# Performance work log

Measured on AMD Instinct MI355X. Metric: run time of the kernel, lower is better.

The kernel has to match this reference:

```python
import jax, jax.numpy as jnp
import numpy as np

D = 256          # feature_dim
H = 4            # num_heads (hard-coded in AdaAttentionalPropagation)
HD = D // H      # per-head dim = 64
L = 6            # number of layers
B, N, M = 2, 2048, 2048
NAMES = ("self", "cross", "self", "cross", "self", "cross")
POOLS = (1, 1, 2, 2, 2, 2)
EPS = 1e-5


def conv1x1(W, b, x):
    # Conv1d kernel_size=1 == pointwise linear over channels: x [B, Cin, N] -> [B, Cout, N]
    return jnp.einsum('oi,bin->bon', W, x) + b[None, :, None]


def inst_norm(x):
    # InstanceNorm1d(affine=False): normalize over spatial dim per (batch, channel)
    mu = jnp.mean(x, axis=-1, keepdims=True)
    var = jnp.var(x, axis=-1, keepdims=True)
    return (x - mu) * jax.lax.rsqrt(var + EPS)


def attn_prop(params, x, source, mask):
    # One AdaAttentionalPropagation layer. x [B,D,Nq], source [B,D,Nk], mask [B,Nq,Nk]
    Wq, bq, Wk, bk, Wv, bv, Wm, bm, W1, b1, W2, b2 = params
    b = x.shape[0]
    q = conv1x1(Wq, bq, x).reshape(b, HD, H, -1)       # [B, hd, H, Nq]
    k = conv1x1(Wk, bk, source).reshape(b, HD, H, -1)  # [B, hd, H, Nk]
    v = conv1x1(Wv, bv, source).reshape(b, HD, H, -1)
    scores = jnp.einsum('bdhn,bdhm->bhnm', q, k) / np.sqrt(HD).astype(np.float32)
    scores = scores * mask[:, None]                     # multiplicative pruned mask
    prob = jax.nn.softmax(scores, axis=-1)              # [B, H, Nq, Nk]
    att = jnp.einsum('bhnm,bdhm->bdhn', prob, v).reshape(b, D, -1)
    message = conv1x1(Wm, bm, att)                      # merge
    y = jnp.concatenate([x, message], axis=1)           # [B, 2D, Nq]
    h = jax.nn.relu(inst_norm(conv1x1(W1, b1, y)))      # MLP_IN hidden
    delta = conv1x1(W2, b2, h)                          # [B, D, Nq]
    return delta, jnp.mean(prob, axis=1)                # prob averaged over heads


def prune(conn, prob, pool, k_cur):
    # update_connections_by_pooling_size: keep top (k_cur // pool) entries per row
    if prob is None or pool == 1:
        return conn, k_cur
    k_new = k_cur // pool
    vals, idxs = jax.lax.top_k(prob, k_new)             # over last axis
    b, n, _ = conn.shape
    new = jnp.zeros_like(conn).at[
        jnp.arange(b)[:, None, None], jnp.arange(n)[None, :, None], idxs
    ].set(jnp.where(vals > 0, 1.0, 0.0).astype(conn.dtype))
    return jax.lax.stop_gradient(new), k_new


def setup_inputs() -> dict:
    key = jax.random.key(0)
    ks = jax.random.split(key, 16)
    s1 = 1.0 / np.sqrt(D)
    s2 = 1.0 / np.sqrt(2 * D)
    return {
        "desc0": jax.random.normal(ks[0], (B, D, N), dtype=jnp.float32),
        "desc1": jax.random.normal(ks[1], (B, D, M), dtype=jnp.float32),
        "Wq": jax.random.normal(ks[2], (L, D, D), dtype=jnp.float32) * s1,
        "bq": jax.random.normal(ks[3], (L, D), dtype=jnp.float32) * 0.01,
        "Wk": jax.random.normal(ks[4], (L, D, D), dtype=jnp.float32) * s1,
        "bk": jax.random.normal(ks[5], (L, D), dtype=jnp.float32) * 0.01,
        "Wv": jax.random.normal(ks[6], (L, D, D), dtype=jnp.float32) * s1,
        "bv": jax.random.normal(ks[7], (L, D), dtype=jnp.float32) * 0.01,
        "Wm": jax.random.normal(ks[8], (L, D, D), dtype=jnp.float32) * s1,
        "bm": jax.random.normal(ks[9], (L, D), dtype=jnp.float32) * 0.01,
        "W1": jax.random.normal(ks[10], (L, 2 * D, 2 * D), dtype=jnp.float32) * s2,
        "b1": jax.random.normal(ks[11], (L, 2 * D), dtype=jnp.float32) * 0.01,
        "W2": jax.random.normal(ks[12], (L, D, 2 * D), dtype=jnp.float32) * s2,
        "b2": jnp.zeros((L, D), dtype=jnp.float32),  # nn.init.constant_(mlp[-1].bias, 0)
    }


def reference(desc0, desc1, Wq, bq, Wk, bk, Wv, bv, Wm, bm, W1, b1, W2, b2):
    b = desc0.shape[0]
    n, m = desc0.shape[2], desc1.shape[2]
    masks = {
        '00': jnp.ones((b, n, n), jnp.float32), '01': jnp.ones((b, n, m), jnp.float32),
        '11': jnp.ones((b, m, m), jnp.float32), '10': jnp.ones((b, m, n), jnp.float32),
    }
    probs = {'00': None, '01': None, '11': None, '10': None}
    kcnt = {'00': n, '01': m, '11': m, '10': n}
    for i in range(L):
        params = (Wq[i], bq[i], Wk[i], bk[i], Wv[i], bv[i],
                  Wm[i], bm[i], W1[i], b1[i], W2[i], b2[i])
        pool = POOLS[i]
        if NAMES[i] == 'cross':
            masks['01'], kcnt['01'] = prune(masks['01'], probs['01'], pool, kcnt['01'])
            delta0, probs['01'] = attn_prop(params, desc0, desc1, masks['01'])
            masks['10'], kcnt['10'] = prune(masks['10'], probs['10'], pool, kcnt['10'])
            delta1, probs['10'] = attn_prop(params, desc1, desc0, masks['10'])
        else:
            masks['00'], kcnt['00'] = prune(masks['00'], probs['00'], pool, kcnt['00'])
            delta0, probs['00'] = attn_prop(params, desc0, desc0, masks['00'])
            masks['11'], kcnt['11'] = prune(masks['11'], probs['11'], pool, kcnt['11'])
            delta1, probs['11'] = attn_prop(params, desc1, desc1, masks['11'])
        desc0 = desc0 + delta0
        desc1 = desc1 + delta1
    return jnp.stack([desc0, desc1])  # [2, B, D, N]
```

## Files before the change

kernel.cpp:

```cpp
#include <hip/hip_runtime.h>
#include <hip/hip_bf16.h>
#include <stdint.h>

#define NPTS 2048
#define MB_ROW 256L
#define MB_B   ((long)NPTS * MB_ROW)
#define MB_T   (2 * MB_B)

typedef __attribute__((ext_vector_type(8))) short bf16x8;
typedef __attribute__((ext_vector_type(4))) float f32x4;
#define MFMA16 __builtin_amdgcn_mfma_f32_16x16x32_bf16

__device__ inline unsigned short f2b(float f) {
  union { float f; unsigned int u; } x; x.f = f;
  unsigned int u = x.u;
  return (unsigned short)((u + 0x7FFFu + ((u >> 16) & 1u)) >> 16);
}
__device__ inline float bfu(unsigned int us) {
  union { unsigned int u; float f; } x; x.u = (us & 0xFFFFu) << 16;
  return x.f;
}
__device__ inline void sp3(float x, unsigned short& h, unsigned short& m, unsigned short& l) {
  h = f2b(x);
  float r1 = x - bfu(h);
  m = f2b(r1);
  l = f2b(r1 - bfu(m));
}
__device__ inline void gld16(const unsigned short* g, unsigned short* l) {
  __builtin_amdgcn_global_load_lds(
      (const __attribute__((address_space(1))) void*)g,
      (__attribute__((address_space(3))) void*)l, 16, 0, 0);
}

#define E_P3  0
#define E_V3  1
#define E_S3  2
#define E_Y3  3
#define E_H   4
#define E_RES 5

template <int EPI>
__global__ __launch_bounds__(256) void t3_k(
    const unsigned short* __restrict__ A, long aps,
    const unsigned short* __restrict__ B, long bps,
    const unsigned short* __restrict__ B2, long b2ps,
    const float* __restrict__ bias,
    void* __restrict__ out,
    const unsigned char* __restrict__ masks,
    int K, int lda, int ldb, int ksplit, long sps,
    int zbase, int xorv, int selfl, int yoff) {
  const int t = threadIdx.x;
  const int z = blockIdx.z;
  const int zg = zbase + z;
  long aoff = 0, boff = 0, b2off = 0;
  if constexpr (EPI == E_P3 || EPI == E_V3) {
    boff = (long)z * 524288;
  } else if constexpr (EPI == E_S3) {
    const int sb = zg >> 2, h = zg & 3;
    aoff = (long)zg * 131072;
    boff = (long)((sb ^ xorv) * 4 + h) * 131072;
  } else if constexpr (EPI == E_Y3) {
    boff = (long)zg * 524288;
  } else if constexpr (EPI == E_H) {
    boff = (long)zg * 524288;
    b2off = (long)z * 524288;
  } else {
    boff = (long)z * 1048576;
  }
  const int n0 = blockIdx.x * 64;
  const int m0 = ((EPI == E_S3) ? yoff : 0) + blockIdx.y * 64;

  __shared__ __align__(16) unsigned short As[3][64 * 64];
  __shared__ __align__(16) unsigned short Bs[3][64 * 64];
  __shared__ unsigned int Ms[128];
  if constexpr (EPI == E_S3) {
    if (t < 128) {
      const int sb = zg >> 2;
      const int type = selfl ? (sb >> 1) : 2 + (sb >> 1);
      const unsigned int* mw =
          (const unsigned int*)(masks + (long)type * MB_T + (long)(sb & 1) * MB_B);
      Ms[t] = mw[(long)(m0 + (t >> 1)) * 64 + (n0 >> 5) + (t & 1)];
    }
  }

  const int w = t >> 6;
  const int L = t & 63;
  const int wm = (w & 1) * 32, wn = (w >> 1) * 32;
  const int lr = t & 15, lk = (t >> 4) & 3;
  const int swr = (lr & 7) << 3;
  const int grow = (L >> 3);
  const int gj = L & 7;

  f32x4 acc[2][2];
#pragma unroll
  for (int i = 0; i < 2; ++i)
#pragma unroll
    for (int j = 0; j < 2; ++j) acc[i][j] = (f32x4){0.f, 0.f, 0.f, 0.f};

  for (int k0 = 0; k0 < K; k0 += 64) {
    const unsigned short* Bsel;
    long bo, bp;
    int kb;
    if (k0 < ksplit) { Bsel = B; bo = boff; bp = bps; kb = k0; }
    else             { Bsel = B2; bo = b2off; bp = b2ps; kb = k0 - ksplit; }
    if (k0) __syncthreads();
#pragma unroll
    for (int pl = 0; pl < 3; ++pl) {
      const unsigned short* Ap = A + (long)pl * aps + aoff;
      const unsigned short* Bp = Bsel + (long)pl * bp + bo;
#pragma unroll
      for (int c = 0; c < 2; ++c) {
        const int rbase = w * 16 + c * 8;
        const int row = rbase + grow;
        const int colA = (gj ^ (row & 7)) << 3;
        gld16(&Ap[(long)(m0 + row) * lda + k0 + colA], &As[pl][rbase * 64]);
        gld16(&Bp[(long)(n0 + row) * ldb + kb + colA], &Bs[pl][rbase * 64]);
      }
    }
    __syncthreads();
#pragma unroll
    for (int kk = 0; kk < 2; ++kk) {
      bf16x8 af[3][2], bf[3][2];
#pragma unroll
      for (int pl = 0; pl < 3; ++pl)
#pragma unroll
        for (int mi = 0; mi < 2; ++mi) {
          af[pl][mi] = *(const bf16x8*)&As[pl][(wm + mi * 16 + lr) * 64 + ((kk * 32 + lk * 8) ^ swr)];
          bf[pl][mi] = *(const bf16x8*)&Bs[pl][(wn + mi * 16 + lr) * 64 + ((kk * 32 + lk * 8) ^ swr)];
        }
#pragma unroll
      for (int mi = 0; mi < 2; ++mi)
#pragma unroll
        for (int ni = 0; ni < 2; ++ni) {
          f32x4 c = acc[mi][ni];
          c = MFMA16(af[2][mi], bf[0][ni], c, 0, 0, 0);
          c = MFMA16(af[0][mi], bf[2][ni], c, 0, 0, 0);
          c = MFMA16(af[1][mi], bf[1][ni], c, 0, 0, 0);
          c = MFMA16(af[1][mi], bf[0][ni], c, 0, 0, 0);
          c = MFMA16(af[0][mi], bf[1][ni], c, 0, 0, 0);
          c = MFMA16(af[0][mi], bf[0][ni], c, 0, 0, 0);
          acc[mi][ni] = c;
        }
    }
  }

  if constexpr (EPI == E_S3) {
    __syncthreads();
    float* ST = (float*)&As[0][0];
#pragma unroll
    for (int mi = 0; mi < 2; ++mi)
#pragma unroll
      for (int ni = 0; ni < 2; ++ni)
#pragma unroll
        for (int r = 0; r < 4; ++r)
          ST[(wm + mi * 16 + lk * 4 + r) * 68 + wn + ni * 16 + lr] = acc[mi][ni][r];
    __syncthreads();
    float* o = (float*)out;
#pragma unroll
    for (int it = 0; it < 4; ++it) {
      const int row = (t >> 4) + it * 16;
      const int col = (t & 15) * 4;
      float4 vv = *(const float4*)&ST[row * 68 + col];
      const unsigned int mw = Ms[row * 2 + (col >> 5)];
      vv.x = ((mw >> ((col + 0) & 31)) & 1u) ? vv.x * 0.125f : 0.f;
      vv.y = ((mw >> ((col + 1) & 31)) & 1u) ? vv.y * 0.125f : 0.f;
      vv.z = ((mw >> ((col + 2) & 31)) & 1u) ? vv.z * 0.125f : 0.f;
      vv.w = ((mw >> ((col + 3) & 31)) & 1u) ? vv.w * 0.125f : 0.f;
      const int rloc = blockIdx.y * 64 + row;
      *(float4*)&o[(long)z * sps + (long)rloc * 2048 + n0 + col] = vv;
    }
    return;
  }

#pragma unroll
  for (int mi = 0; mi < 2; ++mi) {
#pragma unroll
    for (int ni = 0; ni < 2; ++ni) {
      f32x4 a = acc[mi][ni];
      const int cM = m0 + wm + mi * 16 + lk * 4;
      const int pN = n0 + wn + ni * 16 + lr;
      if constexpr (EPI == E_P3) {
        float4 bv4 = *(const float4*)&bias[cM];
        float bb[4] = {bv4.x, bv4.y, bv4.z, bv4.w};
        unsigned short* o = (unsigned short*)out;
        const long b0 = (long)z * 524288 + (long)pN * 64 + (cM >> 2);
#pragma unroll
        for (int r = 0; r < 4; ++r) {
          unsigned short h_, m_, l_;
          sp3(a[r] + bb[r], h_, m_, l_);
          const long ad = b0 + (long)r * 131072;
          o[ad] = h_; o[ad + 2097152] = m_; o[ad + 4194304] = l_;
        }
      } else if constexpr (EPI == E_V3) {
        float4 bv4 = *(const float4*)&bias[cM];
        float bb[4] = {bv4.x, bv4.y, bv4.z, bv4.w};
        unsigned short* o = (unsigned short*)out;
        const long b0 = (long)z * 524288 + (long)(cM >> 2) * 2048 + pN;
#pragma unroll
        for (int r = 0; r < 4; ++r) {
          unsigned short h_, m_, l_;
          sp3(a[r] + bb[r], h_, m_, l_);
          const long ad = b0 + (long)r * 131072;
          o[ad] = h_; o[ad + 2097152] = m_; o[ad + 4194304] = l_;
        }
      } else if constexpr (EPI == E_Y3) {
        float4 bv4 = *(const float4*)&bias[cM];
        float bb[4] = {bv4.x, bv4.y, bv4.z, bv4.w};
        unsigned short* o = (unsigned short*)out;
        ushort4 h4, m4, l4;
        unsigned short* hp = (unsigned short*)&h4;
        unsigned short* mp = (unsigned short*)&m4;
        unsigned short* lp = (unsigned short*)&l4;
#pragma unroll
        for (int r = 0; r < 4; ++r) sp3(a[r] + bb[r], hp[r], mp[r], lp[r]);
        const long b0 = (long)z * 524288 + (long)pN * 256 + cM;
        *(ushort4*)&o[b0] = h4;
        *(ushort4*)&o[b0 + sps] = m4;
        *(ushort4*)&o[b0 + 2 * sps] = l4;
      } else if constexpr (EPI == E_H) {
        *(f32x4*)&((float*)out)[(long)z * 1048576 + (long)pN * 512 + cM] = a;
      } else {
        float4 bv4 = *(const float4*)&bias[cM];
        float* p = &((float*)out)[(long)zg * 524288 + (long)pN * 256 + cM];
        float4 old = *(const float4*)p;
        float4 nw;
        nw.x = old.x + a[0] + bv4.x; nw.y = old.y + a[1] + bv4.y;
        nw.z = old.z + a[2] + bv4.z; nw.w = old.w + a[3] + bv4.w;
        *(float4*)p = nw;
      }
    }
  }
}

__global__ __launch_bounds__(256) void pv3_k(
    const unsigned short* __restrict__ V3, const float* __restrict__ S, long sps,
    const float2* __restrict__ stats, int CH,
    float* __restrict__ part, int zbase, int xorv) {
  const int t = threadIdx.x;
  const int h = blockIdx.z;
  const int kseg = blockIdx.y;
  const int n0 = blockIdx.x * 64;
  const int sb = zbase >> 2;
  const unsigned short* Vb = V3 + (long)((sb ^ xorv) * 4 + h) * 131072;
  const float* Sp = S + (long)h * sps;
  const float2* sth = stats + (long)h * CH;

  __shared__ __align__(16) unsigned short Bs[3][64 * 64];

  const int w = t >> 6;
  const int wm = (w & 1) * 32, wn = (w >> 1) * 32;
  const int lr = t & 15, lk = (t >> 4) & 3;
  const int srow = t >> 3, scol = (t & 7) * 8;
  const int sws = scol ^ ((srow & 7) << 3);
  const int swr = (lr & 7) << 3;

  f32x4 acc[2][2];
#pragma unroll
  for (int i = 0; i < 2; ++i)
#pragma unroll
    for (int j = 0; j < 2; ++j) acc[i][j] = (f32x4){0.f, 0.f, 0.f, 0.f};

  const int kbeg = kseg * 256;
  const float2 st0 = sth[n0 + srow];
  const float2 st1 = sth[n0 + 32 + srow];
  const float* srcA = &Sp[(long)(n0 + srow) * 2048 + kbeg + scol];
  const float* srcB = &Sp[(long)(n0 + 32 + srow) * 2048 + kbeg + scol];

  float4 c0a = *(const float4*)srcA;
  float4 c0b = *(const float4*)(srcA + 4);
  float4 c1a = *(const float4*)srcB;
  float4 c1b = *(const float4*)(srcB + 4);

#pragma unroll
  for (int ki = 0; ki < 4; ++ki) {
    const int k0 = kbeg + ki * 64;
    float4 n0a, n0b, n1a, n1b;
    if (ki < 3) {
      const int off = (ki + 1) * 64;
      n0a = *(const float4*)(srcA + off);
      n0b = *(const float4*)(srcA + off + 4);
      n1a = *(const float4*)(srcB + off);
      n1b = *(const float4*)(srcB + off + 4);
    }
    if (ki) __syncthreads();
    {
      float xs[8] = {c0a.x, c0a.y, c0a.z, c0a.w, c0b.x, c0b.y, c0b.z, c0b.w};
      ushort4 hq[2], mq[2], lq[2];
      unsigned short* hp = (unsigned short*)hq;
      unsigned short* mp = (unsigned short*)mq;
      unsigned short* lp = (unsigned short*)lq;
#pragma unroll
      for (int j = 0; j < 8; ++j) {
        float p = __expf(xs[j] - st0.x) * st0.y;
        sp3(p, hp[j], mp[j], lp[j]);
      }
      *(ushort4*)&Bs[0][srow * 64 + sws] = hq[0];
      *(ushort4*)&Bs[0][srow * 64 + sws + 4] = hq[1];
      *(ushort4*)&Bs[1][srow * 64 + sws] = mq[0];
      *(ushort4*)&Bs[1][srow * 64 + sws + 4] = mq[1];
      *(ushort4*)&Bs[2][srow * 64 + sws] = lq[0];
      *(ushort4*)&Bs[2][srow * 64 + sws + 4] = lq[1];
    }
    {
      float xs[8] = {c1a.x, c1a.y, c1a.z, c1a.w, c1b.x, c1b.y, c1b.z, c1b.w};
      ushort4 hq[2], mq[2], lq[2];
      unsigned short* hp = (unsigned short*)hq;
      unsigned short* mp = (unsigned short*)mq;
      unsigned short* lp = (unsigned short*)lq;
#pragma unroll
      for (int j = 0; j < 8; ++j) {
        float p = __expf(xs[j] - st1.x) * st1.y;
        sp3(p, hp[j], mp[j], lp[j]);
      }
      const int rr = 32 + srow;
      *(ushort4*)&Bs[0][rr * 64 + sws] = hq[0];
      *(ushort4*)&Bs[0][rr * 64 + sws + 4] = hq[1];
      *(ushort4*)&Bs[1][rr * 64 + sws] = mq[0];
      *(ushort4*)&Bs[1][rr * 64 + sws + 4] = mq[1];
      *(ushort4*)&Bs[2][rr * 64 + sws] = lq[0];
      *(ushort4*)&Bs[2][rr * 64 + sws + 4] = lq[1];
    }
    __syncthreads();
#pragma unroll
    for (int kk = 0; kk < 2; ++kk) {
      bf16x8 af[3][2], bf[3][2];
#pragma unroll
      for (int pl = 0; pl < 3; ++pl) {
#pragma unroll
        for (int mi = 0; mi < 2; ++mi) {
          af[pl][mi] = *(const bf16x8*)&Vb[(long)pl * 2097152 +
                                           (long)(wm + mi * 16 + lr) * 2048 + k0 + kk * 32 + lk * 8];
          bf[pl][mi] = *(const bf16x8*)&Bs[pl][(wn + mi * 16 + lr) * 64 + ((kk * 32 + lk * 8) ^ swr)];
        }
      }
#pragma unroll
      for (int mi = 0; mi < 2; ++mi)
#pragma unroll
        for (int ni = 0; ni < 2; ++ni) {
          f32x4 c = acc[mi][ni];
          c = MFMA16(af[2][mi], bf[0][ni], c, 0, 0, 0);
          c = MFMA16(af[0][mi], bf[2][ni], c, 0, 0, 0);
          c = MFMA16(af[1][mi], bf[1][ni], c, 0, 0, 0);
          c = MFMA16(af[1][mi], bf[0][ni], c, 0, 0, 0);
          c = MFMA16(af[0][mi], bf[1][ni], c, 0, 0, 0);
          c = MFMA16(af[0][mi], bf[0][ni], c, 0, 0, 0);
          acc[mi][ni] = c;
        }
    }
    if (ki < 3) { c0a = n0a; c0b = n0b; c1a = n1a; c1b = n1b; }
  }

  float* pp = part + (((long)kseg * 4 + h) * CH) * 64;
#pragma unroll
  for (int mi = 0; mi < 2; ++mi) {
#pragma unroll
    for (int ni = 0; ni < 2; ++ni) {
      const int cM = wm + mi * 16 + lk * 4;
      const int pN = n0 + wn + ni * 16 + lr;
      *(f32x4*)&pp[(long)pN * 64 + cM] = acc[mi][ni];
    }
  }
}

__global__ __launch_bounds__(256) void comb_k(const float* __restrict__ part,
                                              unsigned short* __restrict__ att3,
                                              int CH, int sb, int cb) {
  const int q = threadIdx.x & 63;
  const int g = threadIdx.x >> 6;
  const int nl = blockIdx.x * 4 + g;
  float s[4] = {0.f, 0.f, 0.f, 0.f};
#pragma unroll
  for (int ks = 0; ks < 8; ++ks)
#pragma unroll
    for (int h = 0; h < 4; ++h)
      s[h] += part[(((long)ks * 4 + h) * CH + nl) * 64 + q];
  ushort4 h4, m4, l4;
  unsigned short* hp = (unsigned short*)&h4;
  unsigned short* mp = (unsigned short*)&m4;
  unsigned short* lp = (unsigned short*)&l4;
#pragma unroll
  for (int h = 0; h < 4; ++h) sp3(s[h], hp[h], mp[h], lp[h]);
  const long base = (long)sb * 524288 + (long)(cb + nl) * 256 + 4 * q;
  *(ushort4*)&att3[base] = h4;
  *(ushort4*)&att3[base + 2097152] = m4;
  *(ushort4*)&att3[base + 4194304] = l4;
}

template <int PRUNE>
__global__ __launch_bounds__(256) void softmax_prune_k(
    const float* __restrict__ S, float2* __restrict__ stats,
    unsigned char* __restrict__ masks,
    int knew, int sbG, int cb, int selfl, long sps, int CH) {
  const int lane = threadIdx.x & 63;
  const int wv = threadIdx.x >> 6;
  const int nl = blockIdx.x * 4 + wv;

  __shared__ float meanL[PRUNE ? 4 * 32 * 64 : 1];
  __shared__ int hist[PRUNE ? 4 * 256 : 4];
  float* myMean = PRUNE ? &meanL[(wv * 32) * 64 + lane] : nullptr;

  if constexpr (PRUNE) {
#pragma unroll
    for (int j = 0; j < 32; ++j) myMean[j * 64] = 0.f;
  }

  float mx4[4], ri4[4];
#pragma unroll
  for (int hh = 0; hh < 4; ++hh) {
    const float* row = S + (long)hh * sps + (long)nl * 2048 + lane * 32;
    float xs[32];
#pragma unroll
    for (int e = 0; e < 8; ++e) {
      float4 u = *(const float4*)(row + e * 4);
      xs[e * 4 + 0] = u.x; xs[e * 4 + 1] = u.y;
      xs[e * 4 + 2] = u.z; xs[e * 4 + 3] = u.w;
    }
    float m = xs[0];
#pragma unroll
    for (int j = 1; j < 32; ++j) m = fmaxf(m, xs[j]);
    for (int o = 32; o; o >>= 1) m = fmaxf(m, __shfl_xor(m, o));
    float s = 0.f;
#pragma unroll
    for (int j = 0; j < 32; ++j) { xs[j] = __expf(xs[j] - m); s += xs[j]; }
    for (int o = 32; o; o >>= 1) s += __shfl_xor(s, o);
    const float ri = 1.0f / s;
    mx4[hh] = m; ri4[hh] = ri;
    if constexpr (PRUNE) {
#pragma unroll
      for (int j = 0; j < 32; ++j)
        myMean[j * 64] += 0.25f * (xs[j] * ri);
    }
  }
  if (lane == 0) {
#pragma unroll
    for (int hh = 0; hh < 4; ++hh)
      stats[(long)hh * CH + nl] = make_float2(mx4[hh], ri4[hh]);
  }

  if constexpr (PRUNE) {
    unsigned int key[32];
#pragma unroll
    for (int j = 0; j < 32; ++j) key[j] = __float_as_uint(myMean[j * 64]);

    int* hw = &hist[wv * 256];
    unsigned int pref = 0;
    int kneed = knew;
    for (int pass = 0; pass < 4; ++pass) {
      const int shift = 24 - pass * 8;
      const unsigned int hm = (pass == 0) ? 0u : (0xFFFFFFFFu << (shift + 8));
#pragma unroll
      for (int b = 0; b < 4; ++b) hw[b * 64 + lane] = 0;
      __syncthreads();
#pragma unroll
      for (int j = 0; j < 32; ++j)
        if ((key[j] & hm) == pref) atomicAdd(&hw[(key[j] >> shift) & 255], 1);
      __syncthreads();
      int own[4];
      int tot = 0;
#pragma unroll
      for (int e = 0; e < 4; ++e) { own[e] = hw[lane * 4 + e]; tot += own[e]; }
      int suf = tot;
      for (int o = 1; o < 64; o <<= 1) {
        int tmp = __shfl_down(suf, o);
        if (lane + o < 64) suf += tmp;
      }
      int run = suf - tot;
      int pack = 0;
#pragma unroll
      for (int e = 3; e >= 0; --e) {
        const int Sb = run + own[e];
        if (Sb >= kneed && run < kneed) pack = ((lane * 4 + e) << 20) | (run + 1);
        run = Sb;
      }
      for (int o = 1; o < 64; o <<= 1) pack |= __shfl_xor(pack, o);
      const int bin = pack >> 20;
      const int above = (pack & 0xFFFFF) - 1;
      pref |= ((unsigned int)bin) << shift;
      kneed -= above;
    }
    const unsigned int T = pref;
    const int take = kneed;
    int cnt = 0;
#pragma unroll
    for (int j = 0; j < 32; ++j) cnt += (key[j] == T);
    int pc = cnt;
    for (int o = 1; o < 64; o <<= 1) {
      int tmp = __shfl_up(pc, o);
      if (lane >= o) pc += tmp;
    }
    int base = pc - cnt;
    uchar4 ob;
    unsigned char* obp = (unsigned char*)&ob;
#pragma unroll
    for (int byte = 0; byte < 4; ++byte) {
      unsigned int bb = 0;
#pragma unroll
      for (int e = 0; e < 8; ++e) {
        const int j = byte * 8 + e;
        int sel = 0;
        if (key[j] > T) sel = 1;
        else if (key[j] == T) { if (T > 0u && base < take) sel = 1; base++; }
        bb |= (unsigned int)sel << e;
      }
      obp[byte] = (unsigned char)bb;
    }
    const int type = selfl ? (sbG >> 1) : 2 + (sbG >> 1);
    unsigned char* mb = masks + (long)type * MB_T + (long)(sbG & 1) * MB_B;
    *(uchar4*)&mb[(long)(cb + nl) * MB_ROW + lane * 4] = ob;
  }
}

__global__ __launch_bounds__(256) void inormA_k(const float* __restrict__ H,
                                                float* __restrict__ partial) {
  const int seg = blockIdx.x, sbl = blockIdx.y;
  const float* hp = H + (long)sbl * 1048576;
  const int t = threadIdx.x;
  float s0 = 0.f, q0 = 0.f, s1 = 0.f, q1 = 0.f;
  const int r0 = seg * 64;
  for (int r = r0; r < r0 + 64; ++r) {
    float x0 = hp[(long)r * 512 + t];
    float x1 = hp[(long)r * 512 + t + 256];
    s0 += x0; q0 = fmaf(x0, x0, q0);
    s1 += x1; q1 = fmaf(x1, x1, q1);
  }
  float* pp = partial + ((long)sbl * 32 + seg) * 1024;
  pp[t] = s0; pp[t + 256] = s1;
  pp[512 + t] = q0; pp[512 + t + 256] = q1;
}

__global__ __launch_bounds__(256) void inormB_k(const float* __restrict__ partial,
                                                float* __restrict__ stats2) {
  const int sbl = blockIdx.x;
  const int t = threadIdx.x;
  const float* pp = partial + (long)sbl * 32768;
  float a0 = 0.f, b0 = 0.f, a1 = 0.f, b1 = 0.f;
  for (int seg = 0; seg < 32; ++seg) {
    const float* p = pp + seg * 1024;
    a0 += p[t]; a1 += p[t + 256];
    b0 += p[512 + t]; b1 += p[512 + t + 256];
  }
  float mu0 = a0 * (1.f / 2048.f);
  float mu1 = a1 * (1.f / 2048.f);
  float rs0 = rsqrtf(b0 * (1.f / 2048.f) - mu0 * mu0 + 1e-5f);
  float rs1 = rsqrtf(b1 * (1.f / 2048.f) - mu1 * mu1 + 1e-5f);
  float* st = stats2 + (long)sbl * 1024;
  st[t] = mu0; st[t + 256] = mu1;
  st[512 + t] = rs0; st[512 + t + 256] = rs1;
}

__global__ __launch_bounds__(256) void inormC_k(const float* __restrict__ H,
                                                const float* __restrict__ stats2,
                                                unsigned short* __restrict__ HB,
                                                long hps) {
  const int seg = blockIdx.x, sbl = blockIdx.y;
  const float* hp = H + (long)sbl * 1048576;
  unsigned short* hb = HB + (long)sbl * 1048576;
  const float* st = stats2 + (long)sbl * 1024;
  const int t = threadIdx.x;
  const float mu0 = st[t], mu1 = st[t + 256];
  const float rs0 = st[512 + t], rs1 = st[512 + t + 256];
  const int r0 = seg * 64;
  for (int r = r0; r < r0 + 64; ++r) {
    float x0 = hp[(long)r * 512 + t];
    float x1 = hp[(long)r * 512 + t + 256];
    float o0 = (x0 - mu0) * rs0; o0 = o0 > 0.f ? o0 : 0.f;
    float o1 = (x1 - mu1) * rs1; o1 = o1 > 0.f ? o1 : 0.f;
    unsigned short h_, m_, l_;
    sp3(o0, h_, m_, l_);
    const long ad0 = (long)r * 512 + t;
    hb[ad0] = h_; hb[ad0 + hps] = m_; hb[ad0 + 2 * hps] = l_;
    sp3(o1, h_, m_, l_);
    const long ad1 = ad0 + 256;
    hb[ad1] = h_; hb[ad1 + hps] = m_; hb[ad1 + 2 * hps] = l_;
  }
}

__global__ __launch_bounds__(256) void split6_k(
    const float* __restrict__ q, const float* __restrict__ k,
    const float* __restrict__ v, const float* __restrict__ m,
    const float* __restrict__ w1, const float* __restrict__ w2,
    unsigned short* __restrict__ dst) {
  long i = ((long)blockIdx.x * 256 + threadIdx.x) * 4;
  const float* src;
  long off, base, ps;
  if (i < 262144) {
    int sel = (int)(i >> 16);
    src = sel == 0 ? q : sel == 1 ? k : sel == 2 ? v : m;
    off = i & 65535; base = (long)sel * 196608; ps = 65536;
  } else if (i < 524288) {
    src = w1; off = i - 262144; base = 786432; ps = 262144;
  } else {
    src = w2; off = i - 524288; base = 1572864; ps = 131072;
  }
  float4 vv = *(const float4*)&src[off];
  float xs[4] = {vv.x, vv.y, vv.z, vv.w};
  ushort4 h4, m4, l4;
  unsigned short* hp = (unsigned short*)&h4;
  unsigned short* mp = (unsigned short*)&m4;
  unsigned short* lp = (unsigned short*)&l4;
#pragma unroll
  for (int j = 0; j < 4; ++j) sp3(xs[j], hp[j], mp[j], lp[j]);
  *(ushort4*)&dst[base + off] = h4;
  *(ushort4*)&dst[base + ps + off] = m4;
  *(ushort4*)&dst[base + 2 * ps + off] = l4;
}

__global__ __launch_bounds__(256) void split3_k(const float* __restrict__ src,
                                                unsigned short* __restrict__ dst,
                                                long plane, long n) {
  long i = ((long)blockIdx.x * 256 + threadIdx.x) * 4;
  if (i >= n) return;
  float4 v = *(const float4*)&src[i];
  float xs[4] = {v.x, v.y, v.z, v.w};
  ushort4 h4, m4, l4;
  unsigned short* hp = (unsigned short*)&h4;
  unsigned short* mp = (unsigned short*)&m4;
  unsigned short* lp = (unsigned short*)&l4;
#pragma unroll
  for (int j = 0; j < 4; ++j) sp3(xs[j], hp[j], mp[j], lp[j]);
  *(ushort4*)&dst[i] = h4;
  *(ushort4*)&dst[plane + i] = m4;
  *(ushort4*)&dst[2 * plane + i] = l4;
}

__global__ __launch_bounds__(256) void tin_k(const float* __restrict__ d0,
                                             const float* __restrict__ d1,
                                             float* __restrict__ descT) {
  __shared__ float tl[32][33];
  const int sb = blockIdx.z, s = sb >> 1, b = sb & 1;
  const float* src = (s ? d1 : d0) + (long)b * 524288;
  const int p0 = blockIdx.x * 32, c0 = blockIdx.y * 32;
  const int tx = threadIdx.x & 31, ty = threadIdx.x >> 5;
#pragma unroll
  for (int i = 0; i < 4; ++i)
    tl[ty + i * 8][tx] = src[(long)(c0 + ty + i * 8) * 2048 + p0 + tx];
  __syncthreads();
#pragma unroll
  for (int i = 0; i < 4; ++i)
    descT[(long)sb * 524288 + (long)(p0 + ty + i * 8) * 256 + c0 + tx] = tl[tx][ty + i * 8];
}

__global__ __launch_bounds__(256) void tout_k(const float* __restrict__ descT,
                                              float* __restrict__ out) {
  __shared__ float tl[32][33];
  const int sb = blockIdx.z;
  const int p0 = blockIdx.x * 32, c0 = blockIdx.y * 32;
  const int tx = threadIdx.x & 31, ty = threadIdx.x >> 5;
#pragma unroll
  for (int i = 0; i < 4; ++i)
    tl[ty + i * 8][tx] = descT[(long)sb * 524288 + (long)(p0 + ty + i * 8) * 256 + c0 + tx];
  __syncthreads();
#pragma unroll
  for (int i = 0; i < 4; ++i)
    out[(long)sb * 524288 + (long)(c0 + ty + i * 8) * 2048 + p0 + tx] = tl[tx][ty + i * 8];
}

extern "C" void kernel_launch(void* const* d_in, const int* in_sizes, int n_in,
                              void* d_out, int out_size, void* d_ws, size_t ws_size,
                              hipStream_t stream) {
  (void)in_sizes; (void)n_in; (void)out_size;
  const float* in_d0 = (const float*)d_in[0];
  const float* in_d1 = (const float*)d_in[1];
  const float* Wq = (const float*)d_in[2];
  const float* bq = (const float*)d_in[3];
  const float* Wk = (const float*)d_in[4];
  const float* bk = (const float*)d_in[5];
  const float* Wv = (const float*)d_in[6];
  const float* bv = (const float*)d_in[7];
  const float* Wm = (const float*)d_in[8];
  const float* bm = (const float*)d_in[9];
  const float* W1 = (const float*)d_in[10];
  const float* b1 = (const float*)d_in[11];
  const float* W2 = (const float*)d_in[12];
  const float* b2 = (const float*)d_in[13];
  (void)b1;

  const long region_b = (long)ws_size - 79429632;
  const int CH = (region_b >= 40992L * 2048) ? 2048
               : (region_b >= 40992L * 1024) ? 1024 : 512;
  const int nchunks = 2048 / CH;
  const long sps = (long)CH * 2048;
  const int mb = (region_b >= 4 * 13766656L) ? 4 : (region_b >= 2 * 13766656L) ? 2 : 1;

  uint8_t* w = (uint8_t*)d_ws;
  float* descT          = (float*)w;
  unsigned short* desc3 = (unsigned short*)(w + 8388608);
  unsigned short* Q3    = (unsigned short*)(w + 20971520);
  unsigned short* K3    = (unsigned short*)(w + 33554432);
  unsigned short* V3    = (unsigned short*)(w + 46137344);
  unsigned short* att3  = (unsigned short*)(w + 58720256);
  unsigned short* wbuf  = (unsigned short*)(w + 71303168);
  unsigned char* masks  = w + 75235328;
  uint8_t* region       = w + 79429632;
  float* S              = (float*)region;
  float* part           = (float*)(region + (long)CH * 32768);
  float2* stats         = (float2*)(region + (long)CH * 32768 + (long)CH * 8192);
  unsigned short* msg3  = (unsigned short*)region;
  float* hbuf           = (float*)(region + (long)mb * 3145728);
  unsigned short* hB3   = (unsigned short*)(region + (long)mb * 7340032);
  float* inpart         = (float*)(region + (long)mb * 13631488);
  float* instats        = (float*)(region + (long)mb * 13631488 + (long)mb * 131072);

  const unsigned short* wq3 = wbuf;
  const unsigned short* wk3 = wbuf + 196608;
  const unsigned short* wv3 = wbuf + 393216;
  const unsigned short* wm3 = wbuf + 589824;
  const unsigned short* w13 = wbuf + 786432;
  const unsigned short* w23 = wbuf + 1572864;

  tin_k<<<dim3(64, 8, 4), 256, 0, stream>>>(in_d0, in_d1, descT);
  hipMemsetAsync(masks, 0xFF, 4 * MB_T, stream);

  for (int l = 0; l < 6; ++l) {
    const int selfl = (l % 2 == 0);
    const int xorv = selfl ? 0 : 2;
    const int knew = (l < 2) ? 1024 : (l < 4) ? 512 : 0;

    split6_k<<<dim3(640), 256, 0, stream>>>(Wq + (long)l * 65536, Wk + (long)l * 65536,
                                            Wv + (long)l * 65536, Wm + (long)l * 65536,
                                            W1 + (long)l * 262144, W2 + (long)l * 131072,
                                            wbuf);
    split3_k<<<dim3(2048), 256, 0, stream>>>(descT, desc3, 2097152, 2097152);

    t3_k<E_P3><<<dim3(32, 4, 4), 256, 0, stream>>>(
        wq3, 65536, desc3, 2097152, nullptr, 0, bq + l * 256, Q3, nullptr,
        256, 256, 256, 1 << 30, 0, 0, 0, 0, 0);
    t3_k<E_P3><<<dim3(32, 4, 4), 256, 0, stream>>>(
        wk3, 65536, desc3, 2097152, nullptr, 0, bk + l * 256, K3, nullptr,
        256, 256, 256, 1 << 30, 0, 0, 0, 0, 0);
    t3_k<E_V3><<<dim3(32, 4, 4), 256, 0, stream>>>(
        wv3, 65536, desc3, 2097152, nullptr, 0, bv + l * 256, V3, nullptr,
        256, 256, 256, 1 << 30, 0, 0, 0, 0, 0);

    for (int sb = 0; sb < 4; ++sb) {
      for (int c = 0; c < nchunks; ++c) {
        const int cb = c * CH;
        t3_k<E_S3><<<dim3(32, CH / 64, 4), 256, 0, stream>>>(
            Q3, 2097152, K3, 2097152, nullptr, 0, nullptr, S, masks,
            64, 64, 64, 1 << 30, sps, sb * 4, xorv, selfl, cb);
        if (knew)
          softmax_prune_k<1><<<dim3(CH / 4), 256, 0, stream>>>(S, stats, masks, knew, sb, cb, selfl, sps, CH);
        else
          softmax_prune_k<0><<<dim3(CH / 4), 256, 0, stream>>>(S, stats, masks, knew, sb, cb, selfl, sps, CH);
        pv3_k<<<dim3(CH / 64, 8, 4), 256, 0, stream>>>(V3, S, sps, stats, CH, part, sb * 4, xorv);
        comb_k<<<dim3(CH / 4), 256, 0, stream>>>(part, att3, CH, sb, cb);
      }
    }

    for (int p = 0; p < 4; p += mb) {
      t3_k<E_Y3><<<dim3(32, 4, mb), 256, 0, stream>>>(
          wm3, 65536, att3, 2097152, nullptr, 0, bm + l * 256, msg3, nullptr,
          256, 256, 256, 1 << 30, (long)mb * 524288, p, 0, 0, 0);
      t3_k<E_H><<<dim3(32, 8, mb), 256, 0, stream>>>(
          w13, 262144, desc3, 2097152, msg3, (long)mb * 524288, nullptr, hbuf, nullptr,
          512, 512, 256, 256, 0, p, 0, 0, 0);
      inormA_k<<<dim3(32, mb), 256, 0, stream>>>(hbuf, inpart);
      inormB_k<<<dim3(mb), 256, 0, stream>>>(inpart, instats);
      inormC_k<<<dim3(32, mb), 256, 0, stream>>>(hbuf, instats, hB3, (long)mb * 1048576);
      t3_k<E_RES><<<dim3(32, 4, mb), 256, 0, stream>>>(
          w23, 131072, hB3, (long)mb * 1048576, nullptr, 0, b2 + l * 256, descT, nullptr,
          512, 512, 512, 1 << 30, 0, p, 0, 0, 0);
    }
  }

  tout_k<<<dim3(64, 8, 4), 256, 0, stream>>>(descT, (float*)d_out);
}
```

Before: 2.876 ms.

## Fuse per-tile softmax max/sum stats into score GEMM epilogue

The score GEMM epilogue now computes a per-row, per-64-column-tile max and exp-sum and writes them to a partial buffer that aliases the part scratch space. A small stat_k kernel merges these 32 partials into the row max and inverse sum. The separate softmax pass over S is removed for layers that do not prune, and the prune kernel reuses the precomputed stats. This saves a full read of S whenever no pruning happens, at the cost of extra shuffles and exp evaluations in the GEMM epilogue plus one added small launch.

```diff
diff --git a/kernel.cpp b/kernel.cpp
--- a/kernel.cpp
+++ b/kernel.cpp
@@ -156,6 +156,8 @@
           ST[(wm + mi * 16 + lk * 4 + r) * 68 + wn + ni * 16 + lr] = acc[mi][ni][r];
     __syncthreads();
     float* o = (float*)out;
+    float2* pst = (float2*)const_cast<float*>(bias);
+    const int CHrows = (int)(sps >> 11);
 #pragma unroll
     for (int it = 0; it < 4; ++it) {
       const int row = (t >> 4) + it * 16;
@@ -168,6 +170,15 @@
       vv.w = ((mw >> ((col + 3) & 31)) & 1u) ? vv.w * 0.125f : 0.f;
       const int rloc = blockIdx.y * 64 + row;
       *(float4*)&o[(long)z * sps + (long)rloc * 2048 + n0 + col] = vv;
+      float mx4 = fmaxf(fmaxf(vv.x, vv.y), fmaxf(vv.z, vv.w));
+#pragma unroll
+      for (int oo = 1; oo < 16; oo <<= 1) mx4 = fmaxf(mx4, __shfl_xor(mx4, oo));
+      float e4 = __expf(vv.x - mx4) + __expf(vv.y - mx4) +
+                 __expf(vv.z - mx4) + __expf(vv.w - mx4);
+#pragma unroll
+      for (int oo = 1; oo < 16; oo <<= 1) e4 += __shfl_xor(e4, oo);
+      if ((t & 15) == 0)
+        pst[((long)z * CHrows + rloc) * 32 + blockIdx.x] = make_float2(mx4, e4);
     }
     return;
   }
@@ -232,6 +243,19 @@
   }
 }
 
+__global__ __launch_bounds__(256) void stat_k(const float2* __restrict__ pst,
+                                              float2* __restrict__ stats) {
+  const int idx = blockIdx.x * 256 + threadIdx.x;
+  const float2* p = pst + (long)idx * 32;
+  float m = p[0].x;
+#pragma unroll
+  for (int i = 1; i < 32; ++i) m = fmaxf(m, p[i].x);
+  float s = 0.f;
+#pragma unroll
+  for (int i = 0; i < 32; ++i) s += p[i].y * __expf(p[i].x - m);
+  stats[idx] = make_float2(m, 1.0f / s);
+}
+
 __global__ __launch_bounds__(256) void pv3_k(
     const unsigned short* __restrict__ V3, const float* __restrict__ S, long sps,
     const float2* __restrict__ stats, int CH,
@@ -386,128 +410,104 @@
   *(ushort4*)&att3[base + 4194304] = l4;
 }
 
-template <int PRUNE>
-__global__ __launch_bounds__(256) void softmax_prune_k(
-    const float* __restrict__ S, float2* __restrict__ stats,
+__global__ __launch_bounds__(256) void prune_k(
+    const float* __restrict__ S, const float2* __restrict__ stats,
     unsigned char* __restrict__ masks,
     int knew, int sbG, int cb, int selfl, long sps, int CH) {
   const int lane = threadIdx.x & 63;
   const int wv = threadIdx.x >> 6;
   const int nl = blockIdx.x * 4 + wv;
 
-  __shared__ float meanL[PRUNE ? 4 * 32 * 64 : 1];
-  __shared__ int hist[PRUNE ? 4 * 256 : 4];
-  float* myMean = PRUNE ? &meanL[(wv * 32) * 64 + lane] : nullptr;
-
-  if constexpr (PRUNE) {
-#pragma unroll
-    for (int j = 0; j < 32; ++j) myMean[j * 64] = 0.f;
-  }
-
-  float mx4[4], ri4[4];
+  __shared__ float meanL[4 * 32 * 64];
+  __shared__ int hist[4 * 256];
+  float* myMean = &meanL[(wv * 32) * 64 + lane];
+
+#pragma unroll
+  for (int j = 0; j < 32; ++j) myMean[j * 64] = 0.f;
+
 #pragma unroll
   for (int hh = 0; hh < 4; ++hh) {
+    const float2 st = stats[(long)hh * CH + nl];
     const float* row = S + (long)hh * sps + (long)nl * 2048 + lane * 32;
-    float xs[32];
 #pragma unroll
     for (int e = 0; e < 8; ++e) {
       float4 u = *(const float4*)(row + e * 4);
-      xs[e * 4 + 0] = u.x; xs[e * 4 + 1] = u.y;
-      xs[e * 4 + 2] = u.z; xs[e * 4 + 3] = u.w;
-    }
-    float m = xs[0];
-#pragma unroll
-    for (int j = 1; j < 32; ++j) m = fmaxf(m, xs[j]);
-    for (int o = 32; o; o >>= 1) m = fmaxf(m, __shfl_xor(m, o));
-    float s = 0.f;
-#pragma unroll
-    for (int j = 0; j < 32; ++j) { xs[j] = __expf(xs[j] - m); s += xs[j]; }
-    for (int o = 32; o; o >>= 1) s += __shfl_xor(s, o);
-    const float ri = 1.0f / s;
-    mx4[hh] = m; ri4[hh] = ri;
-    if constexpr (PRUNE) {
-#pragma unroll
-      for (int j = 0; j < 32; ++j)
-        myMean[j * 64] += 0.25f * (xs[j] * ri);
-    }
-  }
-  if (lane == 0) {
-#pragma unroll
-    for (int hh = 0; hh < 4; ++hh)
-      stats[(long)hh * CH + nl] = make_float2(mx4[hh], ri4[hh]);
-  }
-
-  if constexpr (PRUNE) {
-    unsigned int key[32];
-#pragma unroll
-    for (int j = 0; j < 32; ++j) key[j] = __float_as_uint(myMean[j * 64]);
-
-    int* hw = &hist[wv * 256];
-    unsigned int pref = 0;
-    int kneed = knew;
-    for (int pass = 0; pass < 4; ++pass) {
-      const int shift = 24 - pass * 8;
-      const unsigned int hm = (pass == 0) ? 0u : (0xFFFFFFFFu << (shift + 8));
-#pragma unroll
-      for (int b = 0; b < 4; ++b) hw[b * 64 + lane] = 0;
-      __syncthreads();
-#pragma unroll
-      for (int j = 0; j < 32; ++j)
-        if ((key[j] & hm) == pref) atomicAdd(&hw[(key[j] >> shift) & 255], 1);
-      __syncthreads();
-      int own[4];
-      int tot = 0;
-#pragma unroll
-      for (int e = 0; e < 4; ++e) { own[e] = hw[lane * 4 + e]; tot += own[e]; }
-      int suf = tot;
-      for (int o = 1; o < 64; o <<= 1) {
-        int tmp = __shfl_down(suf, o);
-        if (lane + o < 64) suf += tmp;
-      }
-      int run = suf - tot;
-      int pack = 0;
-#pragma unroll
-      for (int e = 3; e >= 0; --e) {
-        const int Sb = run + own[e];
-        if (Sb >= kneed && run < kneed) pack = ((lane * 4 + e) << 20) | (run + 1);
-        run = Sb;
-      }
-      for (int o = 1; o < 64; o <<= 1) pack |= __shfl_xor(pack, o);
-      const int bin = pack >> 20;
-      const int above = (pack & 0xFFFFF) - 1;
-      pref |= ((unsigned int)bin) << shift;
-      kneed -= above;
-    }
-    const unsigned int T = pref;
-    const int take = kneed;
-    int cnt = 0;
-#pragma unroll
-    for (int j = 0; j < 32; ++j) cnt += (key[j] == T);
-    int pc = cnt;
+      myMean[(e * 4 + 0) * 64] += 0.25f * (__expf(u.x - st.x) * st.y);
+      myMean[(e * 4 + 1) * 64] += 0.25f * (__expf(u.y - st.x) * st.y);
+      myMean[(e * 4 + 2) * 64] += 0.25f * (__expf(u.z - st.x) * st.y);
+      myMean[(e * 4 + 3) * 64] += 0.25f * (__expf(u.w - st.x) * st.y);
+    }
+  }
+
+  unsigned int key[32];
+#pragma unroll
+  for (int j = 0; j < 32; ++j) key[j] = __float_as_uint(myMean[j * 64]);
+
+  int* hw = &hist[wv * 256];
+  unsigned int pref = 0;
+  int kneed = knew;
+  for (int pass = 0; pass < 4; ++pass) {
+    const int shift = 24 - pass * 8;
+    const unsigned int hm = (pass == 0) ? 0u : (0xFFFFFFFFu << (shift + 8));
+#pragma unroll
+    for (int b = 0; b < 4; ++b) hw[b * 64 + lane] = 0;
+    __syncthreads();
+#pragma unroll
+    for (int j = 0; j < 32; ++j)
+      if ((key[j] & hm) == pref) atomicAdd(&hw[(key[j] >> shift) & 255], 1);
+    __syncthreads();
+    int own[4];
+    int tot = 0;
+#pragma unroll
+    for (int e = 0; e < 4; ++e) { own[e] = hw[lane * 4 + e]; tot += own[e]; }
+    int suf = tot;
     for (int o = 1; o < 64; o <<= 1) {
-      int tmp = __shfl_up(pc, o);
-      if (lane >= o) pc += tmp;
-    }
-    int base = pc - cnt;
-    uchar4 ob;
-    unsigned char* obp = (unsigned char*)&ob;
-#pragma unroll
-    for (int byte = 0; byte < 4; ++byte) {
-      unsigned int bb = 0;
-#pragma unroll
-      for (int e = 0; e < 8; ++e) {
-        const int j = byte * 8 + e;
-        int sel = 0;
-        if (key[j] > T) sel = 1;
-        else if (key[j] == T) { if (T > 0u && base < take) sel = 1; base++; }
-        bb |= (unsigned int)sel << e;
-      }
-      obp[byte] = (unsigned char)bb;
-    }
-    const int type = selfl ? (sbG >> 1) : 2 + (sbG >> 1);
-    unsigned char* mb = masks + (long)type * MB_T + (long)(sbG & 1) * MB_B;
-    *(uchar4*)&mb[(long)(cb + nl) * MB_ROW + lane * 4] = ob;
-  }
+      int tmp = __shfl_down(suf, o);
+      if (lane + o < 64) suf += tmp;
+    }
+    int run = suf - tot;
+    int pack = 0;
+#pragma unroll
+    for (int e = 3; e >= 0; --e) {
+      const int Sb = run + own[e];
+      if (Sb >= kneed && run < kneed) pack = ((lane * 4 + e) << 20) | (run + 1);
+      run = Sb;
+    }
+    for (int o = 1; o < 64; o <<= 1) pack |= __shfl_xor(pack, o);
+    const int bin = pack >> 20;
+    const int above = (pack & 0xFFFFF) - 1;
+    pref |= ((unsigned int)bin) << shift;
+    kneed -= above;
+  }
+  const unsigned int T = pref;
+  const int take = kneed;
+  int cnt = 0;
+#pragma unroll
+  for (int j = 0; j < 32; ++j) cnt += (key[j] == T);
+  int pc = cnt;
+  for (int o = 1; o < 64; o <<= 1) {
+    int tmp = __shfl_up(pc, o);
+    if (lane >= o) pc += tmp;
+  }
+  int base = pc - cnt;
+  uchar4 ob;
+  unsigned char* obp = (unsigned char*)&ob;
+#pragma unroll
+  for (int byte = 0; byte < 4; ++byte) {
+    unsigned int bb = 0;
+#pragma unroll
+    for (int e = 0; e < 8; ++e) {
+      const int j = byte * 8 + e;
+      int sel = 0;
+      if (key[j] > T) sel = 1;
+      else if (key[j] == T) { if (T > 0u && base < take) sel = 1; base++; }
+      bb |= (unsigned int)sel << e;
+    }
+    obp[byte] = (unsigned char)bb;
+  }
+  const int type = selfl ? (sbG >> 1) : 2 + (sbG >> 1);
+  unsigned char* mb = masks + (long)type * MB_T + (long)(sbG & 1) * MB_B;
+  *(uchar4*)&mb[(long)(cb + nl) * MB_ROW + lane * 4] = ob;
 }
 
 __global__ __launch_bounds__(256) void inormA_k(const float* __restrict__ H,
@@ -694,6 +694,7 @@
   uint8_t* region       = w + 79429632;
   float* S              = (float*)region;
   float* part           = (float*)(region + (long)CH * 32768);
+  float2* pst           = (float2*)part;
   float2* stats         = (float2*)(region + (long)CH * 32768 + (long)CH * 8192);
   unsigned short* msg3  = (unsigned short*)region;
   float* hbuf           = (float*)(region + (long)mb * 3145728);
@@ -736,12 +737,11 @@
       for (int c = 0; c < nchunks; ++c) {
         const int cb = c * CH;
         t3_k<E_S3><<<dim3(32, CH / 64, 4), 256, 0, stream>>>(
-            Q3, 2097152, K3, 2097152, nullptr, 0, nullptr, S, masks,
+            Q3, 2097152, K3, 2097152, nullptr, 0, (const float*)pst, S, masks,
             64, 64, 64, 1 << 30, sps, sb * 4, xorv, selfl, cb);
+        stat_k<<<dim3(4 * CH / 256), 256, 0, stream>>>(pst, stats);
         if (knew)
-          softmax_prune_k<1><<<dim3(CH / 4), 256, 0, stream>>>(S, stats, masks, knew, sb, cb, selfl, sps, CH);
-        else
-          softmax_prune_k<0><<<dim3(CH / 4), 256, 0, stream>>>(S, stats, masks, knew, sb, cb, selfl, sps, CH);
+          prune_k<<<dim3(CH / 4), 256, 0, stream>>>(S, stats, masks, knew, sb, cb, selfl, sps, CH);
         pv3_k<<<dim3(CH / 64, 8, 4), 256, 0, stream>>>(V3, S, sps, stats, CH, part, sb * 4, xorv);
         comb_k<<<dim3(CH / 4), 256, 0, stream>>>(part, att3, CH, sb, cb);
       }
```

Measured after the change: 3.235 ms. 12.5% more time.
